# Performance work log

Hardware: AMD Instinct MI355X
Metric: run time of the kernel (lower is better)

The kernel has to match this reference:

```python
import jax, jax.numpy as jnp
import numpy as np

B, Q, LE, D, P, A = 8, 32, 128, 512, 32, 128


def setup_inputs() -> dict:
    key = jax.random.key(0)
    ks = jax.random.split(key, 8)
    exp_tokens = jax.random.normal(ks[0], (B, Q, LE, D), dtype=jnp.float32)
    exp_mask = jax.random.randint(ks[1], (B, Q, LE), 0, 2, dtype=jnp.int32)
    s_j = jax.random.normal(ks[2], (B, P, D), dtype=jnp.float32)
    req_mask = jax.random.randint(ks[3], (B, P), 0, 2, dtype=jnp.int32)
    sc = 1.0 / np.sqrt(D)
    Ws_w = jax.random.normal(ks[4], (A, D), dtype=jnp.float32) * sc
    Ws_b = jax.random.normal(ks[5], (A,), dtype=jnp.float32) * 0.01
    U_w = jax.random.normal(ks[6], (A, D), dtype=jnp.float32) * sc
    v_w = jax.random.normal(ks[7], (1, A), dtype=jnp.float32) * (1.0 / np.sqrt(A))
    return {"exp_tokens": exp_tokens, "exp_mask": exp_mask, "s_j": s_j,
            "req_mask": req_mask, "Ws_w": Ws_w, "Ws_b": Ws_b, "U_w": U_w, "v_w": v_w}


def reference(exp_tokens, exp_mask, s_j, req_mask, Ws_w, Ws_b, U_w, v_w):
    # ws: (B,P,A); uh: (B,Q,Le,A)
    ws = jnp.einsum('bpd,ad->bpa', s_j, Ws_w) + Ws_b
    uh = jnp.einsum('bqtd,ad->bqta', exp_tokens, U_w)
    # broadcast add -> (B,Q,P,Le,A), tanh, project with v -> (B,Q,P,Le)
    scored = jnp.tanh(uh[:, :, None, :, :] + ws[:, None, :, None, :])
    e = jnp.einsum('bqpta,a->bqpt', scored, v_w[0])
    tok_mask = exp_mask[:, :, None, :]  # (B,Q,1,Le) broadcast over P
    e = jnp.where(tok_mask == 0, jnp.float32(-1e9), e)
    # joint softmax over Q*Le per (b,p)
    e_t = jnp.transpose(e, (0, 2, 1, 3)).reshape(e.shape[0], e.shape[2], -1)
    a = jax.nn.softmax(e_t, axis=-1).reshape(e.shape[0], e.shape[2], e.shape[1], e.shape[3])
    a = jnp.transpose(a, (0, 2, 1, 3))  # (B,Q,P,Le)
    s_rlk = jnp.einsum('bqpt,bqtd->bqpd', a, exp_tokens)
    rmask = req_mask[:, None, :, None].astype(s_rlk.dtype)
    return s_rlk * rmask
```

## Files before the change

kernel.cpp:

```cpp
#include <hip/hip_runtime.h>
#include <hip/hip_bf16.h>

#define B_  8
#define Q_  32
#define LE_ 128
#define D_  512
#define P_  32
#define A_  128

typedef __attribute__((ext_vector_type(8))) short short8_t;
typedef __attribute__((ext_vector_type(4))) float floatx4_t;

typedef const __attribute__((address_space(1))) unsigned int glb_uint;
typedef __attribute__((address_space(3))) unsigned int lds_uint;
#define GLD16(g, s) __builtin_amdgcn_global_load_lds((glb_uint*)(g), (lds_uint*)(s), 16, 0, 0)

__device__ __forceinline__ short f2bf(float x) {
    unsigned u = __float_as_uint(x);
    unsigned r = (u + 0x7fffu + ((u >> 16) & 1u)) >> 16;
    return (short)r;
}
__device__ __forceinline__ float bf2f(short s) {
    return __uint_as_float(((unsigned)(unsigned short)s) << 16);
}
__device__ __forceinline__ short8_t cvt8(float4 a, float4 b) {
    short8_t s;
    s[0] = f2bf(a.x); s[1] = f2bf(a.y); s[2] = f2bf(a.z); s[3] = f2bf(a.w);
    s[4] = f2bf(b.x); s[5] = f2bf(b.y); s[6] = f2bf(b.z); s[7] = f2bf(b.w);
    return s;
}

__global__ __launch_bounds__(256) void prep_kernel(
    const float* __restrict__ X, const float* __restrict__ W,
    const float* __restrict__ s_j, const float* __restrict__ Ws_w,
    const float* __restrict__ Ws_b,
    short* __restrict__ Xb, short* __restrict__ Wb,
    float* __restrict__ EW, float* __restrict__ gsums) {
    __shared__ float s_row[D_];
    int blk = blockIdx.x;
    int tid = threadIdx.x;
    if (blk < 256) {
        int bp = blk;
        if (blk == 0) gsums[tid] = 0.0f;
        const float* src = s_j + (size_t)bp * D_;
        for (int i = tid; i < D_; i += 256) s_row[i] = src[i];
        __syncthreads();
        if (tid < 128) {
            int a = tid;
            const float4* w4 = (const float4*)(Ws_w + (size_t)a * D_);
            const float4* s4 = (const float4*)s_row;
            float acc = 0.0f;
#pragma unroll 8
            for (int i = 0; i < D_ / 4; ++i) {
                float4 w = w4[i];
                acc += w.x * s4[i].x + w.y * s4[i].y + w.z * s4[i].z + w.w * s4[i].w;
            }
            EW[bp * A_ + a] = __expf(2.0f * (acc + Ws_b[a]));
        }
        return;
    }
    int cb = blk - 256;
    if (cb < 2048) {
        size_t g = (size_t)cb * 1024 + tid;
        float4 v[8];
#pragma unroll
        for (int u = 0; u < 4; ++u) {
            const float4* s4 = (const float4*)(X + (g + (size_t)u * 256) * 8);
            v[u * 2]     = s4[0];
            v[u * 2 + 1] = s4[1];
        }
#pragma unroll
        for (int u = 0; u < 4; ++u)
            *(short8_t*)(Xb + (g + (size_t)u * 256) * 8) = cvt8(v[u * 2], v[u * 2 + 1]);
    } else {
        size_t g = (size_t)(cb - 2048) * 256 + tid;
        const float4* s4 = (const float4*)(W + g * 8);
        float4 a = s4[0], b = s4[1];
        *(short8_t*)(Wb + g * 8) = cvt8(a, b);
    }
}

#define EUP_ 136
#define EWP_ 132
#define WPP_ 136

__global__ __launch_bounds__(512, 1) void score_kernel(
    const short* __restrict__ Xb, const short* __restrict__ Wb,
    const float* __restrict__ EW, const float* __restrict__ v_w,
    const int* __restrict__ exp_mask, float* __restrict__ gsums,
    short* __restrict__ wglob) {
    __shared__ short uA[128 * EUP_];
    __shared__ float ew_s[32 * EWP_];
    __shared__ short w_s[32 * WPP_];
    __shared__ float n2v[128];
    __shared__ int   mask_s[128];

    int bq = blockIdx.x;
    int b  = bq >> 5;
    int tid = threadIdx.x;
    int wave = tid >> 6, lane = tid & 63;
    int qd = lane >> 4, lr = lane & 15;

    short* As = uA;
    short* Bs = uA + 8192;

    int m0 = (wave >> 1) * 32, n0 = (wave & 1) * 64;
    int cA = lane & 7;
    int row0 = wave * 16 + (lane >> 3);

    floatx4_t acc[2][4];
#pragma unroll
    for (int i = 0; i < 2; ++i)
#pragma unroll
        for (int j = 0; j < 4; ++j) acc[i][j] = (floatx4_t){0.f, 0.f, 0.f, 0.f};

    for (int kt = 0; kt < 8; ++kt) {
        int k0 = kt * 64;
        __syncthreads();
#pragma unroll
        for (int u = 0; u < 2; ++u) {
            int m = row0 + u * 8;
            GLD16(Xb + (size_t)(bq * 128 + m) * D_ + k0 + ((cA ^ (m & 7)) * 8),
                  As + (wave * 2 + u) * 512);
        }
#pragma unroll
        for (int u = 0; u < 2; ++u) {
            int n = row0 + u * 8;
            GLD16(Wb + (size_t)n * D_ + k0 + ((cA ^ (n & 7)) * 8),
                  Bs + (wave * 2 + u) * 512);
        }
        __syncthreads();
#pragma unroll
        for (int ks = 0; ks < 2; ++ks) {
            int cr = (ks * 4 + qd) ^ (lr & 7);
            short8_t af[2], bfr[4];
#pragma unroll
            for (int i = 0; i < 2; ++i)
                af[i] = *(const short8_t*)(As + (m0 + i * 16 + lr) * 64 + cr * 8);
#pragma unroll
            for (int j = 0; j < 4; ++j)
                bfr[j] = *(const short8_t*)(Bs + (n0 + j * 16 + lr) * 64 + cr * 8);
#pragma unroll
            for (int i = 0; i < 2; ++i)
#pragma unroll
                for (int j = 0; j < 4; ++j)
                    acc[i][j] = __builtin_amdgcn_mfma_f32_16x16x32_bf16(af[i], bfr[j], acc[i][j], 0, 0, 0);
        }
    }
    __syncthreads();

#pragma unroll
    for (int i = 0; i < 2; ++i)
#pragma unroll
        for (int j = 0; j < 4; ++j)
#pragma unroll
            for (int r = 0; r < 4; ++r) {
                int t = m0 + i * 16 + qd * 4 + r;
                int a = n0 + j * 16 + lr;
                uA[t * EUP_ + a] = f2bf(__expf(2.0f * acc[i][j][r]));
            }
#pragma unroll
    for (int u = 0; u < 2; ++u) {
        int c = tid * 2 + u;
        int p = c >> 5, seg = c & 31;
        *(float4*)&ew_s[p * EWP_ + seg * 4] =
            *(const float4*)&EW[(size_t)(b * P_ + p) * A_ + seg * 4];
    }
    if (tid < 32) {
        float4 v = *(const float4*)(v_w + tid * 4);
        v.x *= -2.0f; v.y *= -2.0f; v.z *= -2.0f; v.w *= -2.0f;
        *(float4*)&n2v[tid * 4] = v;
    }
    if (tid < 128) mask_s[tid] = exp_mask[bq * LE_ + tid];
    __syncthreads();

    {
        int t = tid & 127, pg = tid >> 7;
        float acc8[8];
#pragma unroll
        for (int j = 0; j < 8; ++j) acc8[j] = 0.0f;
        for (int a8 = 0; a8 < 16; ++a8) {
            short8_t e8 = *(const short8_t*)&uA[t * EUP_ + a8 * 8];
            float eu[8];
#pragma unroll
            for (int k = 0; k < 8; ++k) eu[k] = bf2f(e8[k]);
            float4 nv0 = *(const float4*)&n2v[a8 * 8];
            float4 nv1 = *(const float4*)&n2v[a8 * 8 + 4];
            float nv[8] = {nv0.x, nv0.y, nv0.z, nv0.w, nv1.x, nv1.y, nv1.z, nv1.w};
#pragma unroll
            for (int j = 0; j < 8; ++j) {
                int p = pg * 8 + j;
                float4 w0 = *(const float4*)&ew_s[p * EWP_ + a8 * 8];
                float4 w1 = *(const float4*)&ew_s[p * EWP_ + a8 * 8 + 4];
                float ww[8] = {w0.x, w0.y, w0.z, w0.w, w1.x, w1.y, w1.z, w1.w};
#pragma unroll
                for (int k = 0; k < 8; ++k)
                    acc8[j] = fmaf(nv[k], __builtin_amdgcn_rcpf(fmaf(eu[k], ww[k], 1.0f)), acc8[j]);
            }
        }
        int mk = mask_s[t];
        short* wg = wglob + (size_t)bq * (P_ * LE_);
#pragma unroll
        for (int j = 0; j < 8; ++j) {
            float ee = mk ? __expf(acc8[j]) : 0.0f;
            short v = f2bf(ee);
            w_s[(pg * 8 + j) * WPP_ + t] = v;
            wg[(pg * 8 + j) * LE_ + t] = v;
        }
    }
    __syncthreads();

    if (tid < 256) {
        int p = tid >> 3, seg = tid & 7;
        const short* src = w_s + p * WPP_ + seg * 16;
        float s = 0.0f;
#pragma unroll
        for (int k = 0; k < 16; ++k) s += bf2f(src[k]);
        s += __shfl_xor(s, 1);
        s += __shfl_xor(s, 2);
        s += __shfl_xor(s, 4);
        if (seg == 0) atomicAdd(&gsums[b * P_ + p], s);
    }
}

__global__ __launch_bounds__(512, 4) void pv_kernel(
    const short* __restrict__ Xb, const short* __restrict__ wglob,
    const float* __restrict__ gsums, const int* __restrict__ req_mask,
    float* __restrict__ out) {
    __shared__ short pvB[128 * EUP_];
    __shared__ float rm_s[32];

    int blk = blockIdx.x;
    int bq = blk >> 2, chunk = blk & 3;
    int b = bq >> 5;
    int d0 = chunk * 128;
    int tid = threadIdx.x;
    int wave = tid >> 6, lane = tid & 63;
    int qd = lane >> 4, lr = lane & 15;

    if (tid < 32) {
        int bp = b * P_ + tid;
        float g = gsums[bp];
        rm_s[tid] = req_mask[bp] ? __builtin_amdgcn_rcpf(g) : 0.0f;
    }

    const short* wg = wglob + (size_t)bq * (P_ * LE_);
    short8_t afv[2][4];
#pragma unroll
    for (int i = 0; i < 2; ++i)
#pragma unroll
        for (int ks = 0; ks < 4; ++ks)
            afv[i][ks] = *(const short8_t*)&wg[(i * 16 + lr) * LE_ + ks * 32 + qd * 8];

    int tt = tid >> 2, dseg = (tid & 3) * 32;
    const short8_t* g = (const short8_t*)(Xb + (size_t)(bq * 128 + tt) * D_ + d0 + dseg);
    short8_t xs0 = g[0], xs1 = g[1], xs2 = g[2], xs3 = g[3];
#pragma unroll
    for (int e = 0; e < 8; ++e) {
        pvB[(dseg + 0 + e) * EUP_ + tt]  = xs0[e];
        pvB[(dseg + 8 + e) * EUP_ + tt]  = xs1[e];
        pvB[(dseg + 16 + e) * EUP_ + tt] = xs2[e];
        pvB[(dseg + 24 + e) * EUP_ + tt] = xs3[e];
    }
    __syncthreads();

    floatx4_t accp[2];
    accp[0] = (floatx4_t){0.f, 0.f, 0.f, 0.f};
    accp[1] = (floatx4_t){0.f, 0.f, 0.f, 0.f};
#pragma unroll
    for (int ks = 0; ks < 4; ++ks) {
        short8_t bfr = *(const short8_t*)&pvB[(wave * 16 + lr) * EUP_ + ks * 32 + qd * 8];
        accp[0] = __builtin_amdgcn_mfma_f32_16x16x32_bf16(afv[0][ks], bfr, accp[0], 0, 0, 0);
        accp[1] = __builtin_amdgcn_mfma_f32_16x16x32_bf16(afv[1][ks], bfr, accp[1], 0, 0, 0);
    }
#pragma unroll
    for (int i = 0; i < 2; ++i)
#pragma unroll
        for (int r = 0; r < 4; ++r) {
            int p = i * 16 + qd * 4 + r;
            __builtin_nontemporal_store(
                accp[i][r] * rm_s[p],
                &out[((size_t)bq * P_ + p) * D_ + d0 + wave * 16 + lr]);
        }
}

extern "C" void kernel_launch(void* const* d_in, const int* in_sizes, int n_in,
                              void* d_out, int out_size, void* d_ws, size_t ws_size,
                              hipStream_t stream) {
    const float* exp_tokens = (const float*)d_in[0];
    const int*   exp_mask   = (const int*)d_in[1];
    const float* s_j        = (const float*)d_in[2];
    const int*   req_mask   = (const int*)d_in[3];
    const float* Ws_w       = (const float*)d_in[4];
    const float* Ws_b       = (const float*)d_in[5];
    const float* U_w        = (const float*)d_in[6];
    const float* v_w        = (const float*)d_in[7];
    float* out = (float*)d_out;

    float* EW    = (float*)d_ws;
    float* gsums = EW + B_ * P_ * A_;
    short* Xb    = (short*)(gsums + 256);
    short* Wb    = Xb + (size_t)B_ * Q_ * LE_ * D_;
    short* wglob = Wb + (size_t)A_ * D_;

    prep_kernel<<<dim3(256 + 2048 + 32), dim3(256), 0, stream>>>(
        exp_tokens, U_w, s_j, Ws_w, Ws_b, Xb, Wb, EW, gsums);
    score_kernel<<<dim3(B_ * Q_), dim3(512), 0, stream>>>(
        Xb, Wb, EW, v_w, exp_mask, gsums, wglob);
    pv_kernel<<<dim3(B_ * Q_ * 4), dim3(512), 0, stream>>>(
        Xb, wglob, gsums, req_mask, out);
}
```

Measured before the change: 156.3 us.

## Fuse fp32-to-bf16 conversion of tokens into score and PV kernels

The separate pass that converted exp_tokens to a bf16 workspace copy is removed. The score kernel now reads fp32 tokens directly, converts them in registers and writes them to LDS, using double-buffered LDS with a register prefetch of the next k-tile. The PV kernel also reads fp32 tokens and converts them on the fly. This removes a full write and reread of the bf16 copy, in exchange for reading fp32 twice and doing conversion work inside the compute kernels.

```diff
diff --git a/kernel.cpp b/kernel.cpp
--- a/kernel.cpp
+++ b/kernel.cpp
@@ -31,10 +31,10 @@
 }
 
 __global__ __launch_bounds__(256) void prep_kernel(
-    const float* __restrict__ X, const float* __restrict__ W,
+    const float* __restrict__ W,
     const float* __restrict__ s_j, const float* __restrict__ Ws_w,
     const float* __restrict__ Ws_b,
-    short* __restrict__ Xb, short* __restrict__ Wb,
+    short* __restrict__ Wb,
     float* __restrict__ EW, float* __restrict__ gsums) {
     __shared__ float s_row[D_];
     int blk = blockIdx.x;
@@ -59,25 +59,10 @@
         }
         return;
     }
-    int cb = blk - 256;
-    if (cb < 2048) {
-        size_t g = (size_t)cb * 1024 + tid;
-        float4 v[8];
-#pragma unroll
-        for (int u = 0; u < 4; ++u) {
-            const float4* s4 = (const float4*)(X + (g + (size_t)u * 256) * 8);
-            v[u * 2]     = s4[0];
-            v[u * 2 + 1] = s4[1];
-        }
-#pragma unroll
-        for (int u = 0; u < 4; ++u)
-            *(short8_t*)(Xb + (g + (size_t)u * 256) * 8) = cvt8(v[u * 2], v[u * 2 + 1]);
-    } else {
-        size_t g = (size_t)(cb - 2048) * 256 + tid;
-        const float4* s4 = (const float4*)(W + g * 8);
-        float4 a = s4[0], b = s4[1];
-        *(short8_t*)(Wb + g * 8) = cvt8(a, b);
-    }
+    size_t g = (size_t)(blk - 256) * 256 + tid;
+    const float4* s4 = (const float4*)(W + g * 8);
+    float4 a = s4[0], b = s4[1];
+    *(short8_t*)(Wb + g * 8) = cvt8(a, b);
 }
 
 #define EUP_ 136
@@ -85,11 +70,11 @@
 #define WPP_ 136
 
 __global__ __launch_bounds__(512, 1) void score_kernel(
-    const short* __restrict__ Xb, const short* __restrict__ Wb,
+    const float* __restrict__ X, const short* __restrict__ Wb,
     const float* __restrict__ EW, const float* __restrict__ v_w,
     const int* __restrict__ exp_mask, float* __restrict__ gsums,
     short* __restrict__ wglob) {
-    __shared__ short uA[128 * EUP_];
+    __shared__ short uS[32768];
     __shared__ float ew_s[32 * EWP_];
     __shared__ short w_s[32 * WPP_];
     __shared__ float n2v[128];
@@ -101,12 +86,17 @@
     int wave = tid >> 6, lane = tid & 63;
     int qd = lane >> 4, lr = lane & 15;
 
-    short* As = uA;
-    short* Bs = uA + 8192;
-
     int m0 = (wave >> 1) * 32, n0 = (wave & 1) * 64;
-    int cA = lane & 7;
-    int row0 = wave * 16 + (lane >> 3);
+    int cB = lane & 7;
+    int rowB0 = wave * 16 + (lane >> 3);
+
+    int rowA = tid >> 2;
+    int ksg  = (tid & 3) * 16;
+    int cb0  = (tid & 3) * 2;
+    int wcb0 = (cb0 ^ (rowA & 7)) * 8;
+    int wcb1 = ((cb0 + 1) ^ (rowA & 7)) * 8;
+    const float* xrow = X + (size_t)(bq * 128 + rowA) * D_ + ksg;
+    int aoff = rowA * 64;
 
     floatx4_t acc[2][4];
 #pragma unroll
@@ -114,40 +104,57 @@
 #pragma unroll
         for (int j = 0; j < 4; ++j) acc[i][j] = (floatx4_t){0.f, 0.f, 0.f, 0.f};
 
+    {
+        const float4* xs = (const float4*)xrow;
+        float4 a0 = xs[0], a1 = xs[1], a2 = xs[2], a3 = xs[3];
+        *(short8_t*)(uS + aoff + wcb0) = cvt8(a0, a1);
+        *(short8_t*)(uS + aoff + wcb1) = cvt8(a2, a3);
+#pragma unroll
+        for (int u = 0; u < 2; ++u) {
+            int n = rowB0 + u * 8;
+            GLD16(Wb + (size_t)n * D_ + ((cB ^ (n & 7)) * 8),
+                  uS + 16384 + (wave * 2 + u) * 512);
+        }
+    }
+    __syncthreads();
+
     for (int kt = 0; kt < 8; ++kt) {
-        int k0 = kt * 64;
-        __syncthreads();
-#pragma unroll
-        for (int u = 0; u < 2; ++u) {
-            int m = row0 + u * 8;
-            GLD16(Xb + (size_t)(bq * 128 + m) * D_ + k0 + ((cA ^ (m & 7)) * 8),
-                  As + (wave * 2 + u) * 512);
-        }
-#pragma unroll
-        for (int u = 0; u < 2; ++u) {
-            int n = row0 + u * 8;
-            GLD16(Wb + (size_t)n * D_ + k0 + ((cA ^ (n & 7)) * 8),
-                  Bs + (wave * 2 + u) * 512);
-        }
-        __syncthreads();
+        int cur = (kt & 1) << 13;
+        int nxt = cur ^ 8192;
+        float4 xv0, xv1, xv2, xv3;
+        if (kt < 7) {
+            const float4* xs = (const float4*)(xrow + (kt + 1) * 64);
+            xv0 = xs[0]; xv1 = xs[1]; xv2 = xs[2]; xv3 = xs[3];
+#pragma unroll
+            for (int u = 0; u < 2; ++u) {
+                int n = rowB0 + u * 8;
+                GLD16(Wb + (size_t)n * D_ + (kt + 1) * 64 + ((cB ^ (n & 7)) * 8),
+                      uS + 16384 + nxt + (wave * 2 + u) * 512);
+            }
+        }
 #pragma unroll
         for (int ks = 0; ks < 2; ++ks) {
             int cr = (ks * 4 + qd) ^ (lr & 7);
             short8_t af[2], bfr[4];
 #pragma unroll
             for (int i = 0; i < 2; ++i)
-                af[i] = *(const short8_t*)(As + (m0 + i * 16 + lr) * 64 + cr * 8);
+                af[i] = *(const short8_t*)(uS + cur + (m0 + i * 16 + lr) * 64 + cr * 8);
 #pragma unroll
             for (int j = 0; j < 4; ++j)
-                bfr[j] = *(const short8_t*)(Bs + (n0 + j * 16 + lr) * 64 + cr * 8);
+                bfr[j] = *(const short8_t*)(uS + 16384 + cur + (n0 + j * 16 + lr) * 64 + cr * 8);
 #pragma unroll
             for (int i = 0; i < 2; ++i)
 #pragma unroll
                 for (int j = 0; j < 4; ++j)
                     acc[i][j] = __builtin_amdgcn_mfma_f32_16x16x32_bf16(af[i], bfr[j], acc[i][j], 0, 0, 0);
         }
-    }
-    __syncthreads();
+        __syncthreads();
+        if (kt < 7) {
+            *(short8_t*)(uS + nxt + aoff + wcb0) = cvt8(xv0, xv1);
+            *(short8_t*)(uS + nxt + aoff + wcb1) = cvt8(xv2, xv3);
+            __syncthreads();
+        }
+    }
 
 #pragma unroll
     for (int i = 0; i < 2; ++i)
@@ -157,7 +164,7 @@
             for (int r = 0; r < 4; ++r) {
                 int t = m0 + i * 16 + qd * 4 + r;
                 int a = n0 + j * 16 + lr;
-                uA[t * EUP_ + a] = f2bf(__expf(2.0f * acc[i][j][r]));
+                uS[t * EUP_ + a] = f2bf(__expf(2.0f * acc[i][j][r]));
             }
 #pragma unroll
     for (int u = 0; u < 2; ++u) {
@@ -180,7 +187,7 @@
 #pragma unroll
         for (int j = 0; j < 8; ++j) acc8[j] = 0.0f;
         for (int a8 = 0; a8 < 16; ++a8) {
-            short8_t e8 = *(const short8_t*)&uA[t * EUP_ + a8 * 8];
+            short8_t e8 = *(const short8_t*)&uS[t * EUP_ + a8 * 8];
             float eu[8];
 #pragma unroll
             for (int k = 0; k < 8; ++k) eu[k] = bf2f(e8[k]);
@@ -224,7 +231,7 @@
 }
 
 __global__ __launch_bounds__(512, 4) void pv_kernel(
-    const short* __restrict__ Xb, const short* __restrict__ wglob,
+    const float* __restrict__ X, const short* __restrict__ wglob,
     const float* __restrict__ gsums, const int* __restrict__ req_mask,
     float* __restrict__ out) {
     __shared__ short pvB[128 * EUP_];
@@ -253,8 +260,10 @@
             afv[i][ks] = *(const short8_t*)&wg[(i * 16 + lr) * LE_ + ks * 32 + qd * 8];
 
     int tt = tid >> 2, dseg = (tid & 3) * 32;
-    const short8_t* g = (const short8_t*)(Xb + (size_t)(bq * 128 + tt) * D_ + d0 + dseg);
-    short8_t xs0 = g[0], xs1 = g[1], xs2 = g[2], xs3 = g[3];
+    const float4* g4 = (const float4*)(X + (size_t)(bq * 128 + tt) * D_ + d0 + dseg);
+    float4 f0 = g4[0], f1 = g4[1], f2 = g4[2], f3 = g4[3];
+    float4 f4 = g4[4], f5 = g4[5], f6 = g4[6], f7 = g4[7];
+    short8_t xs0 = cvt8(f0, f1), xs1 = cvt8(f2, f3), xs2 = cvt8(f4, f5), xs3 = cvt8(f6, f7);
 #pragma unroll
     for (int e = 0; e < 8; ++e) {
         pvB[(dseg + 0 + e) * EUP_ + tt]  = xs0[e];
@@ -299,14 +308,13 @@
 
     float* EW    = (float*)d_ws;
     float* gsums = EW + B_ * P_ * A_;
-    short* Xb    = (short*)(gsums + 256);
-    short* Wb    = Xb + (size_t)B_ * Q_ * LE_ * D_;
+    short* Wb    = (short*)(gsums + 256);
     short* wglob = Wb + (size_t)A_ * D_;
 
-    prep_kernel<<<dim3(256 + 2048 + 32), dim3(256), 0, stream>>>(
-        exp_tokens, U_w, s_j, Ws_w, Ws_b, Xb, Wb, EW, gsums);
+    prep_kernel<<<dim3(256 + 32), dim3(256), 0, stream>>>(
+        U_w, s_j, Ws_w, Ws_b, Wb, EW, gsums);
     score_kernel<<<dim3(B_ * Q_), dim3(512), 0, stream>>>(
-        Xb, Wb, EW, v_w, exp_mask, gsums, wglob);
+        exp_tokens, Wb, EW, v_w, exp_mask, gsums, wglob);
     pv_kernel<<<dim3(B_ * Q_ * 4), dim3(512), 0, stream>>>(
-        Xb, wglob, gsums, req_mask, out);
-}
+        exp_tokens, wglob, gsums, req_mask, out);
+}
```

New measurement: 161.3 us. 1.03x slower.
